# Kernel tuning notes

Hardware: AMD Instinct MI355X
Metric: run time of the kernel (lower is better)

The kernel has to match this reference:

```python
import jax, jax.numpy as jnp
import numpy as np

LAMBDA_SOFTMAX = 9.0
LAMBDA_LSE = 6.0
EPS = 1e-8
LEAKY_SLOPE = 0.1


def setup_inputs() -> dict:
    key = jax.random.key(0)
    k1, k2, k3, k4 = jax.random.split(key, 4)
    B, R, L, D = 256, 36, 40, 1024  # n_image=n_caption=B, n_regions, max_words, embed
    return {
        'pool_img': jax.random.normal(k1, (B, D), jnp.float32),
        'img_emb': jax.random.normal(k2, (B, R, D), jnp.float32),
        'pool_txt': jax.random.normal(k3, (B, D), jnp.float32),
        'cap_emb': jax.random.normal(k4, (B, L, D), jnp.float32),
    }


def _l2norm(x, axis):
    return x / (jnp.sqrt(jnp.sum(x * x, axis=axis, keepdims=True)) + EPS)


def _lse_reduce(m):
    # mul_(lambda_lse).exp_() ; sum over singleton dim ; log / lambda_lse
    return jnp.log(jnp.exp(m * LAMBDA_LSE)) / LAMBDA_LSE


def _text_score_one(cap_i, txt_poo_i, images):
    # cap_i: (L, d) query; images: (B, R, d) context. clipped_l2norm variant.
    attn = jnp.einsum('brd,ld->brl', images, cap_i)            # (B, R, L)
    attn = jax.nn.leaky_relu(attn, LEAKY_SLOPE)
    attn = _l2norm(attn, axis=2)                               # l2norm over queryL
    attn = jnp.swapaxes(attn, 1, 2)                            # (B, L, R)
    attn = jax.nn.softmax(attn * LAMBDA_SOFTMAX, axis=-1)      # softmax over regions
    wctx = jnp.einsum('blr,brd->bld', attn, images)            # (B, L, d)
    w12 = jnp.einsum('bld,d->bl', wctx, txt_poo_i)
    w1 = jnp.sqrt(jnp.sum(txt_poo_i * txt_poo_i))
    w2 = jnp.sqrt(jnp.sum(wctx * wctx, axis=2))
    sim = w12 / jnp.maximum(w1 * w2, EPS)                      # (B, L)
    return _lse_reduce(jnp.mean(sim, axis=1))                  # (B,)


def _image_score_one(cap_i, img_emb, img_poo):
    # query: img_emb (B, R, d); context: cap_i (L, d) broadcast over B.
    attn = jnp.einsum('ld,brd->blr', cap_i, img_emb)           # (B, L, R)
    attn = jax.nn.leaky_relu(attn, LEAKY_SLOPE)
    attn = _l2norm(attn, axis=2)                               # l2norm over regions
    attn = jnp.swapaxes(attn, 1, 2)                            # (B, R, L)
    attn = jax.nn.softmax(attn * LAMBDA_SOFTMAX, axis=-1)      # softmax over words
    wctx = jnp.einsum('brl,ld->brd', attn, cap_i)              # (B, R, d)
    w12 = jnp.einsum('brd,bd->br', wctx, img_poo)
    w1 = jnp.sqrt(jnp.sum(img_poo * img_poo, axis=1, keepdims=True))  # (B,1)
    w2 = jnp.sqrt(jnp.sum(wctx * wctx, axis=2))                # (B, R)
    sim = w12 / jnp.maximum(w1 * w2, EPS)
    return _lse_reduce(jnp.mean(sim, axis=1))                  # (B,)


def reference(pool_img, img_emb, pool_txt, cap_emb):
    # scores_t2i: loop over captions -> vmap; result (n_cap, n_image) -> transpose
    t2i = jax.vmap(_text_score_one, in_axes=(0, 0, None))(cap_emb, pool_txt, img_emb).T
    i2t = jax.vmap(_image_score_one, in_axes=(0, None, None))(cap_emb, img_emb, pool_img).T
    base = pool_img @ pool_txt.T
    return t2i + i2t + base
```

## Files before the change

kernel.cpp:

```cpp
#include <hip/hip_runtime.h>

typedef unsigned short u16;
typedef __attribute__((ext_vector_type(8))) short bf16x8;
typedef __attribute__((ext_vector_type(4))) float f32x4;

#define D_EMB 1024
#define NBAT  256
#define AS1 __attribute__((address_space(1)))
#define AS3 __attribute__((address_space(3)))

__device__ __forceinline__ u16 f2bf(float f){
    unsigned int u = __float_as_uint(f);
    unsigned int r = (u + 0x7fffu + ((u >> 16) & 1u)) >> 16;
    return (u16)r;
}
__device__ __forceinline__ float leaky(float x){ return x > 0.f ? x : 0.1f * x; }

__device__ __forceinline__ unsigned pack2(float a, float b){
    return (__float_as_uint(a) >> 16) | (__float_as_uint(b) & 0xffff0000u);
}
__device__ __forceinline__ float unpk_lo(unsigned p){ return __uint_as_float(p << 16); }
__device__ __forceinline__ float unpk_hi(unsigned p){ return __uint_as_float(p & 0xffff0000u); }

__global__ void pack_kernel(const float* __restrict__ pool_img, const float* __restrict__ img_emb,
                            const float* __restrict__ pool_txt, const float* __restrict__ cap_emb,
                            u16* __restrict__ imgw, u16* __restrict__ capw){
    int row = blockIdx.x;
    const float* src; u16* dst;
    if (row < NBAT * 37){
        int e = row / 37, rr = row - e * 37;
        src = (rr < 36) ? (img_emb + ((size_t)e * 36 + rr) * D_EMB) : (pool_img + (size_t)e * D_EMB);
        dst = imgw + (size_t)row * D_EMB;
    } else {
        int r2 = row - NBAT * 37;
        int e = r2 / 41, rr = r2 - e * 41;
        src = (rr < 40) ? (cap_emb + ((size_t)e * 40 + rr) * D_EMB) : (pool_txt + (size_t)e * D_EMB);
        dst = capw + (size_t)r2 * D_EMB;
    }
    int t = threadIdx.x;
    float4 v = ((const float4*)src)[t];
    unsigned long long pk = (unsigned long long)f2bf(v.x)
        | ((unsigned long long)f2bf(v.y) << 16)
        | ((unsigned long long)f2bf(v.z) << 32)
        | ((unsigned long long)f2bf(v.w) << 48);
    *(unsigned long long*)(dst + (size_t)t * 4) = pk;
}

__global__ void norm_kernel(const float* __restrict__ pool_img, const float* __restrict__ pool_txt,
                            float* __restrict__ w1i, float* __restrict__ w1t){
    __shared__ float red[256];
    int v = blockIdx.x;
    const float* src = (v < 256) ? (pool_img + (size_t)v * D_EMB)
                                 : (pool_txt + (size_t)(v - 256) * D_EMB);
    int t = threadIdx.x;
    float4 x = ((const float4*)src)[t];
    red[t] = x.x*x.x + x.y*x.y + x.z*x.z + x.w*x.w;
    __syncthreads();
    for (int off = 128; off > 0; off >>= 1){
        if (t < off) red[t] += red[t + off];
        __syncthreads();
    }
    if (t == 0){
        float n = sqrtf(red[0]);
        if (v < 256) w1i[v] = n; else w1t[v - 256] = n;
    }
}

__launch_bounds__(256, 2)
__global__ void gram_kernel(const u16* __restrict__ imgw, const u16* __restrict__ capw,
                            float* __restrict__ G, float* __restrict__ H){
    __shared__ __align__(16) char gsm[6144];
    int blk = blockIdx.x;
    int tid = threadIdx.x, lane = tid & 63;
    int wave = __builtin_amdgcn_readfirstlane(tid >> 6);
    int frow = lane & 15, q = lane >> 4;

    const u16* E; float* Gout; int R;
    if (blk < NBAT){ E = imgw + (size_t)blk * 37 * D_EMB; Gout = G + (size_t)blk * 1296; R = 36; }
    else { int b = blk - NBAT; E = capw + (size_t)b * 41 * D_EMB; Gout = H + (size_t)b * 1600; R = 40; }

    {
        uint4 z = {0u,0u,0u,0u};
        for (int off = tid * 16; off < 6144; off += 4096) *(uint4*)(gsm + off) = z;
    }

    const u16* gsrc[2]; int goff[2]; bool gval[2];
    #pragma unroll
    for (int j = 0; j < 2; ++j){
        int g = wave + j * 4;
        gval[j] = false; gsrc[j] = E; goff[j] = 0;
        if (g < 6){
            int kk = g / 3, t = g - kk * 3;
            int row = t * 16 + frow;
            gsrc[j] = E + (size_t)row * D_EMB + kk * 32 + q * 8;
            goff[j] = g * 1024;
            gval[j] = (row < R);
        }
    }

    int wm = wave >> 1, wn = wave & 1;
    int nTm = wm ? 1 : 2, nTn = wn ? 1 : 2;
    f32x4 acc[2][2];
    #pragma unroll
    for (int a = 0; a < 2; ++a)
        #pragma unroll
        for (int b = 0; b < 2; ++b) acc[a][b] = (f32x4){0.f,0.f,0.f,0.f};

    for (int c = 0; c < 16; ++c){
        __syncthreads();
        #pragma unroll
        for (int j = 0; j < 2; ++j){
            if (gval[j]){
                __builtin_amdgcn_global_load_lds(
                    (const AS1 void*)(const void*)(gsrc[j] + c * 64),
                    (AS3 void*)(void*)(gsm + goff[j] + lane * 16),
                    16, 0, 0);
            }
        }
        __syncthreads();
        #pragma unroll
        for (int kk = 0; kk < 2; ++kk){
            bf16x8 fA[2], fB[2];
            #pragma unroll
            for (int mi = 0; mi < 2; ++mi)
                if (mi < nTm) fA[mi] = *(const bf16x8*)(gsm + ((kk * 3 + (wm + mi * 2)) * 64 + lane) * 16);
            #pragma unroll
            for (int ni = 0; ni < 2; ++ni)
                if (ni < nTn) fB[ni] = *(const bf16x8*)(gsm + ((kk * 3 + (wn + ni * 2)) * 64 + lane) * 16);
            #pragma unroll
            for (int mi = 0; mi < 2; ++mi)
                if (mi < nTm)
                    #pragma unroll
                    for (int ni = 0; ni < 2; ++ni)
                        if (ni < nTn)
                            acc[mi][ni] = __builtin_amdgcn_mfma_f32_16x16x32_bf16(
                                fA[mi], fB[ni], acc[mi][ni], 0, 0, 0);
        }
    }

    #pragma unroll
    for (int mi = 0; mi < 2; ++mi){
        if (mi < nTm){
            int tm = wm + mi * 2;
            #pragma unroll
            for (int ni = 0; ni < 2; ++ni){
                if (ni < nTn){
                    int tn = wn + ni * 2;
                    int col = tn * 16 + frow;
                    if (col < R){
                        #pragma unroll
                        for (int g = 0; g < 4; ++g){
                            int row = tm * 16 + q * 4 + g;
                            if (row < R) Gout[row * R + col] = acc[mi][ni][g];
                        }
                    }
                }
            }
        }
    }
}

__launch_bounds__(256, 5)
__global__ void fused_kernel(const u16* __restrict__ imgw, const u16* __restrict__ capw,
                             const float* __restrict__ G, const float* __restrict__ H,
                             const float* __restrict__ w1i, const float* __restrict__ w1t,
                             float* __restrict__ out){
    __shared__ __align__(16) char smem[26624];
    float* Call = (float*)smem;
    float* rnb  = (float*)(smem + 25160);
    float* cnb  = (float*)(smem + 25736);

    int tid  = threadIdx.x;
    int lane = tid & 63;
    int wave = __builtin_amdgcn_readfirstlane(tid >> 6);
    int frow = lane & 15, q = lane >> 4;

    int lin = blockIdx.x;
    int xcd = lin & 7;
    int s   = lin >> 3;
    int b_t = (xcd << 4) | (s & 15);
    int i_t = s >> 4;
    int b0 = b_t * 2, i0 = i_t * 2;
    const u16* Ag = imgw + (size_t)b0 * 37 * D_EMB;
    const u16* Bg = capw + (size_t)i0 * 41 * D_EMB;

    {
        uint4 z = {0u,0u,0u,0u};
        for (int off = tid * 16; off < 22528; off += 4096) *(uint4*)(smem + off) = z;
    }

    const u16* gsrc[6]; int goff[6]; bool gval[6];
    #pragma unroll
    for (int j = 0; j < 6; ++j){
        int g = wave + j * 4;
        gval[j] = false; gsrc[j] = Ag; goff[j] = 0;
        if (g < 22){
            if (g < 10){
                int tm = g % 5, kk = g / 5;
                int row = tm * 16 + frow;
                gsrc[j] = Ag + (size_t)row * D_EMB + kk * 32 + q * 8;
                goff[j] = g * 1024;
                gval[j] = (row < 74);
            } else {
                int gb = g - 10;
                int tn = gb % 6, kk = gb / 6;
                int row = tn * 16 + frow;
                gsrc[j] = Bg + (size_t)row * D_EMB + kk * 32 + q * 8;
                goff[j] = 10240 + gb * 1024;
                gval[j] = (row < 82);
            }
        }
    }

    int wm = wave >> 1, wn = wave & 1;
    int nTm = wm ? 2 : 3;
    f32x4 acc[3][3];
    #pragma unroll
    for (int aa = 0; aa < 3; ++aa)
        #pragma unroll
        for (int bb = 0; bb < 3; ++bb) acc[aa][bb] = (f32x4){0.f, 0.f, 0.f, 0.f};

    for (int c = 0; c < 16; ++c){
        __syncthreads();
        #pragma unroll
        for (int j = 0; j < 6; ++j){
            if (gval[j]){
                __builtin_amdgcn_global_load_lds(
                    (const AS1 void*)(const void*)(gsrc[j] + c * 64),
                    (AS3 void*)(void*)(smem + goff[j] + lane * 16),
                    16, 0, 0);
            }
        }
        __syncthreads();
        #pragma unroll
        for (int kk = 0; kk < 2; ++kk){
            bf16x8 bfr[3];
            #pragma unroll
            for (int ni = 0; ni < 3; ++ni){
                int tn = wn + ni * 2;
                bfr[ni] = *(const bf16x8*)(smem + 10240 + ((kk * 6 + tn) * 64 + lane) * 16);
            }
            #pragma unroll
            for (int mi = 0; mi < 3; ++mi){
                if (mi < nTm){
                    int tm = wm + mi * 2;
                    bf16x8 af = *(const bf16x8*)(smem + ((kk * 5 + tm) * 64 + lane) * 16);
                    #pragma unroll
                    for (int ni = 0; ni < 3; ++ni){
                        acc[mi][ni] = __builtin_amdgcn_mfma_f32_16x16x32_bf16(
                            af, bfr[ni], acc[mi][ni], 0, 0, 0);
                    }
                }
            }
        }
    }
    __syncthreads();

    #pragma unroll
    for (int mi = 0; mi < 3; ++mi){
        if (mi < nTm){
            int tm = wm + mi * 2;
            #pragma unroll
            for (int ni = 0; ni < 3; ++ni){
                int tn = wn + ni * 2;
                int col = tn * 16 + frow;
                int rbase = tm * 16 + q * 4;
                if (col < 82){
                    #pragma unroll
                    for (int g = 0; g < 4; ++g){
                        int rowc = rbase + g;
                        if (rowc < 74) Call[rowc * 85 + col] = acc[mi][ni][g];
                    }
                }
            }
        }
    }
    __syncthreads();

    int pb = wave >> 1, pi = wave & 1;
    int bg = b0 + pb, ig = i0 + pi;
    const float* Sv = Call + (pb * 37) * 85 + pi * 41;
    const float* Gb = G + (size_t)bg * 1296;
    const float* Hi = H + (size_t)ig * 1600;

    {
        int r0 = (lane < 36) ? lane : 35;
        float s2 = 0.f;
        #pragma unroll
        for (int l = 0; l < 40; ++l){ float x = leaky(Sv[r0 * 85 + l]); s2 = fmaf(x, x, s2); }
        if (lane < 36) rnb[wave * 36 + lane] = 1.f / (sqrtf(s2) + 1e-8f);
    }
    float t2i_sum;
    {
        int lc = (lane < 40) ? lane : 39;
        unsigned up[18];
        float dd = 0.f, num = 0.f;
        #pragma unroll
        for (int r = 0; r < 36; r += 2){
            float x0 = leaky(Sv[r * 85 + lc]);
            float e0 = __expf(9.0f * x0 * rnb[wave * 36 + r]);
            float x1 = leaky(Sv[(r + 1) * 85 + lc]);
            float e1 = __expf(9.0f * x1 * rnb[wave * 36 + r + 1]);
            dd += e0 + e1;
            num = fmaf(e0, Sv[r * 85 + 40], fmaf(e1, Sv[(r + 1) * 85 + 40], num));
            up[r >> 1] = pack2(e0, e1);
        }
        float zz = 0.f;
        #pragma unroll
        for (int rr = 0; rr < 36; ++rr){
            float urr = (rr & 1) ? unpk_hi(up[rr >> 1]) : unpk_lo(up[rr >> 1]);
            float t = 0.f;
            #pragma unroll
            for (int r2 = rr + 1; r2 < 36; ++r2){
                float ur2 = (r2 & 1) ? unpk_hi(up[r2 >> 1]) : unpk_lo(up[r2 >> 1]);
                t = fmaf(Gb[rr * 36 + r2], ur2, t);
            }
            zz += (2.f * t + Gb[rr * 36 + rr] * urr) * urr;
        }
        float w2s = sqrtf(fmaxf(zz, 0.f));
        float sim = num / fmaxf(w1t[ig] * w2s, 1e-8f);
        sim = (lane < 40) ? sim : 0.f;
        #pragma unroll
        for (int off = 32; off > 0; off >>= 1) sim += __shfl_down(sim, off);
        t2i_sum = sim;
    }

    {
        int l0 = (lane < 40) ? lane : 39;
        float s2 = 0.f;
        #pragma unroll
        for (int r = 0; r < 36; ++r){ float x = leaky(Sv[r * 85 + l0]); s2 = fmaf(x, x, s2); }
        if (lane < 40) cnb[wave * 40 + lane] = 1.f / (sqrtf(s2) + 1e-8f);
    }
    float i2t_sum;
    {
        int rc = (lane < 36) ? lane : 35;
        unsigned vp[20];
        float dd = 0.f, num = 0.f;
        #pragma unroll
        for (int l = 0; l < 40; l += 2){
            float x0 = leaky(Sv[rc * 85 + l]);
            float e0 = __expf(9.0f * x0 * cnb[wave * 40 + l]);
            float x1 = leaky(Sv[rc * 85 + l + 1]);
            float e1 = __expf(9.0f * x1 * cnb[wave * 40 + l + 1]);
            dd += e0 + e1;
            num = fmaf(e0, Sv[36 * 85 + l], fmaf(e1, Sv[36 * 85 + l + 1], num));
            vp[l >> 1] = pack2(e0, e1);
        }
        float zz = 0.f;
        #pragma unroll
        for (int ll = 0; ll < 40; ++ll){
            float vll = (ll & 1) ? unpk_hi(vp[ll >> 1]) : unpk_lo(vp[ll >> 1]);
            float t = 0.f;
            #pragma unroll
            for (int l2 = ll + 1; l2 < 40; ++l2){
                float vl2 = (l2 & 1) ? unpk_hi(vp[l2 >> 1]) : unpk_lo(vp[l2 >> 1]);
                t = fmaf(Hi[ll * 40 + l2], vl2, t);
            }
            zz += (2.f * t + Hi[ll * 40 + ll] * vll) * vll;
        }
        float w2s = sqrtf(fmaxf(zz, 0.f));
        float sim = num / fmaxf(w1i[bg] * w2s, 1e-8f);
        sim = (lane < 36) ? sim : 0.f;
        #pragma unroll
        for (int off = 32; off > 0; off >>= 1) sim += __shfl_down(sim, off);
        i2t_sum = sim;
    }

    if (lane == 0)
        out[bg * 256 + ig] = t2i_sum * (1.f / 40.f) + i2t_sum * (1.f / 36.f) + Sv[36 * 85 + 40];
}

extern "C" void kernel_launch(void* const* d_in, const int* in_sizes, int n_in,
                              void* d_out, int out_size, void* d_ws, size_t ws_size,
                              hipStream_t stream){
    const float* pool_img = (const float*)d_in[0];
    const float* img_emb  = (const float*)d_in[1];
    const float* pool_txt = (const float*)d_in[2];
    const float* cap_emb  = (const float*)d_in[3];
    float* out = (float*)d_out;

    char* ws = (char*)d_ws;
    size_t o = 0;
    u16* imgw = (u16*)(ws + o);  o += (size_t)256 * 37 * 1024 * 2;
    u16* capw = (u16*)(ws + o);  o += (size_t)256 * 41 * 1024 * 2;
    float* G  = (float*)(ws + o); o += (size_t)256 * 36 * 36 * 4;
    float* H  = (float*)(ws + o); o += (size_t)256 * 40 * 40 * 4;
    float* w1i = (float*)(ws + o); o += 1024;
    float* w1t = (float*)(ws + o); o += 1024;

    pack_kernel<<<19968, 256, 0, stream>>>(pool_img, img_emb, pool_txt, cap_emb, imgw, capw);
    norm_kernel<<<512, 256, 0, stream>>>(pool_img, pool_txt, w1i, w1t);
    gram_kernel<<<512, 256, 0, stream>>>(imgw, capw, G, H);
    fused_kernel<<<16384, 256, 0, stream>>>(imgw, capw, G, H, w1i, w1t, out);
}
```

Before: 753.4 us.

## Compute softmax-weight quadratic forms with MFMA against bf16-padded Gram matrices

The per-lane scalar quadratic form u^T G u (and v^T H v), which read fp32 Gram entries from global memory inside a triangular unrolled loop, is replaced by MFMA products. The Gram matrices are stored as zero-padded 48x64 bf16 tiles, and the packed exp weights are staged through a per-wave LDS buffer as the B operand. This cuts the scalar FMA count and the global load traffic in the hot epilogue. In exchange it adds LDS staging, bf16 rounding of G/H, a larger shared-memory footprint that may reduce occupancy, and reliance on compiler-only barriers for intra-wave LDS ordering.

```diff
diff --git a/kernel.cpp b/kernel.cpp
--- a/kernel.cpp
+++ b/kernel.cpp
@@ -8,6 +8,7 @@
 #define NBAT  256
 #define AS1 __attribute__((address_space(1)))
 #define AS3 __attribute__((address_space(3)))
+#define MEMBAR() asm volatile("" ::: "memory")
 
 __device__ __forceinline__ u16 f2bf(float f){
     unsigned int u = __float_as_uint(f);
@@ -68,19 +69,23 @@
 
 __launch_bounds__(256, 2)
 __global__ void gram_kernel(const u16* __restrict__ imgw, const u16* __restrict__ capw,
-                            float* __restrict__ G, float* __restrict__ H){
+                            u16* __restrict__ Gp, u16* __restrict__ Hp){
     __shared__ __align__(16) char gsm[6144];
     int blk = blockIdx.x;
     int tid = threadIdx.x, lane = tid & 63;
     int wave = __builtin_amdgcn_readfirstlane(tid >> 6);
     int frow = lane & 15, q = lane >> 4;
 
-    const u16* E; float* Gout; int R;
-    if (blk < NBAT){ E = imgw + (size_t)blk * 37 * D_EMB; Gout = G + (size_t)blk * 1296; R = 36; }
-    else { int b = blk - NBAT; E = capw + (size_t)b * 41 * D_EMB; Gout = H + (size_t)b * 1600; R = 40; }
-
-    {
-        uint4 z = {0u,0u,0u,0u};
+    const u16* E; u16* Gout; int R;
+    if (blk < NBAT){ E = imgw + (size_t)blk * 37 * D_EMB; Gout = Gp + (size_t)blk * 3072; R = 36; }
+    else { int b = blk - NBAT; E = capw + (size_t)b * 41 * D_EMB; Gout = Hp + (size_t)b * 3072; R = 40; }
+
+    for (int idx = tid; idx < 3072; idx += 256){
+        int row = idx >> 6, col = idx & 63;
+        if (row >= R || col >= R) Gout[idx] = 0;
+    }
+
+    {   uint4 z = {0u,0u,0u,0u};
         for (int off = tid * 16; off < 6144; off += 4096) *(uint4*)(gsm + off) = z;
     }
 
@@ -151,7 +156,7 @@
                         #pragma unroll
                         for (int g = 0; g < 4; ++g){
                             int row = tm * 16 + q * 4 + g;
-                            if (row < R) Gout[row * R + col] = acc[mi][ni][g];
+                            if (row < R) Gout[row * 64 + col] = f2bf(acc[mi][ni][g]);
                         }
                     }
                 }
@@ -162,13 +167,11 @@
 
 __launch_bounds__(256, 5)
 __global__ void fused_kernel(const u16* __restrict__ imgw, const u16* __restrict__ capw,
-                             const float* __restrict__ G, const float* __restrict__ H,
+                             const u16* __restrict__ Gp, const u16* __restrict__ Hp,
                              const float* __restrict__ w1i, const float* __restrict__ w1t,
                              float* __restrict__ out){
-    __shared__ __align__(16) char smem[26624];
+    __shared__ __align__(16) char smem[32768];
     float* Call = (float*)smem;
-    float* rnb  = (float*)(smem + 25160);
-    float* cnb  = (float*)(smem + 25736);
 
     int tid  = threadIdx.x;
     int lane = tid & 63;
@@ -187,6 +190,8 @@
     {
         uint4 z = {0u,0u,0u,0u};
         for (int off = tid * 16; off < 22528; off += 4096) *(uint4*)(smem + off) = z;
+        *(uint4*)(smem + 24576 + tid * 32)      = z;
+        *(uint4*)(smem + 24576 + tid * 32 + 16) = z;
     }
 
     const u16* gsrc[6]; int goff[6]; bool gval[6];
@@ -269,7 +274,7 @@
                     #pragma unroll
                     for (int g = 0; g < 4; ++g){
                         int rowc = rbase + g;
-                        if (rowc < 74) Call[rowc * 85 + col] = acc[mi][ni][g];
+                        if (rowc < 74) Call[rowc * 83 + col] = acc[mi][ni][g];
                     }
                 }
             }
@@ -279,88 +284,155 @@
 
     int pb = wave >> 1, pi = wave & 1;
     int bg = b0 + pb, ig = i0 + pi;
-    const float* Sv = Call + (pb * 37) * 85 + pi * 41;
-    const float* Gb = G + (size_t)bg * 1296;
-    const float* Hi = H + (size_t)ig * 1600;
+    const float* Sv = Call + (pb * 37) * 83 + pi * 41;
+    const u16* Gb = Gp + (size_t)bg * 3072;
+    const u16* Hb = Hp + (size_t)ig * 3072;
+    char*  pbuf  = smem + 24576 + wave * 2048;
+    float* pnorm = (float*)pbuf;
+
+    float t2i_sum, i2t_sum;
 
     {
         int r0 = (lane < 36) ? lane : 35;
         float s2 = 0.f;
         #pragma unroll
-        for (int l = 0; l < 40; ++l){ float x = leaky(Sv[r0 * 85 + l]); s2 = fmaf(x, x, s2); }
-        if (lane < 36) rnb[wave * 36 + lane] = 1.f / (sqrtf(s2) + 1e-8f);
-    }
-    float t2i_sum;
+        for (int l = 0; l < 40; ++l){ float x = leaky(Sv[r0 * 83 + l]); s2 = fmaf(x, x, s2); }
+        if (lane < 36) pnorm[lane] = 1.f / (sqrtf(s2) + 1e-8f);
+        MEMBAR();
+    }
     {
         int lc = (lane < 40) ? lane : 39;
         unsigned up[18];
-        float dd = 0.f, num = 0.f;
+        float num = 0.f;
         #pragma unroll
         for (int r = 0; r < 36; r += 2){
-            float x0 = leaky(Sv[r * 85 + lc]);
-            float e0 = __expf(9.0f * x0 * rnb[wave * 36 + r]);
-            float x1 = leaky(Sv[(r + 1) * 85 + lc]);
-            float e1 = __expf(9.0f * x1 * rnb[wave * 36 + r + 1]);
-            dd += e0 + e1;
-            num = fmaf(e0, Sv[r * 85 + 40], fmaf(e1, Sv[(r + 1) * 85 + 40], num));
+            float x0 = leaky(Sv[r * 83 + lc]);
+            float e0 = __expf(9.0f * x0 * pnorm[r]);
+            float x1 = leaky(Sv[(r + 1) * 83 + lc]);
+            float e1 = __expf(9.0f * x1 * pnorm[r + 1]);
+            num = fmaf(e0, Sv[r * 83 + 40], fmaf(e1, Sv[(r + 1) * 83 + 40], num));
             up[r >> 1] = pack2(e0, e1);
         }
-        float zz = 0.f;
-        #pragma unroll
-        for (int rr = 0; rr < 36; ++rr){
-            float urr = (rr & 1) ? unpk_hi(up[rr >> 1]) : unpk_lo(up[rr >> 1]);
-            float t = 0.f;
-            #pragma unroll
-            for (int r2 = rr + 1; r2 < 36; ++r2){
-                float ur2 = (r2 & 1) ? unpk_hi(up[r2 >> 1]) : unpk_lo(up[r2 >> 1]);
-                t = fmaf(Gb[rr * 36 + r2], ur2, t);
-            }
-            zz += (2.f * t + Gb[rr * 36 + rr] * urr) * urr;
-        }
-        float w2s = sqrtf(fmaxf(zz, 0.f));
-        float sim = num / fmaxf(w1t[ig] * w2s, 1e-8f);
+        MEMBAR();
+        float zzp[3];
+        #pragma unroll
+        for (int ni = 0; ni < 3; ++ni){
+            if (lane < 40 && (lane >> 4) == ni){
+                int fr = lane & 15;
+                #pragma unroll
+                for (int qq = 0; qq < 4; ++qq){
+                    uint4 w = {up[qq * 4], up[qq * 4 + 1], up[qq * 4 + 2], up[qq * 4 + 3]};
+                    *(uint4*)(pbuf + (qq * 16 + fr) * 16) = w;
+                }
+                uint4 w1 = {up[16], up[17], 0u, 0u};
+                *(uint4*)(pbuf + 1024 + fr * 16) = w1;
+            }
+            MEMBAR();
+            uint4 tb0 = *(const uint4*)(pbuf + lane * 16);
+            uint4 tb1 = *(const uint4*)(pbuf + 1024 + lane * 16);
+            bf16x8 B0 = __builtin_bit_cast(bf16x8, tb0);
+            bf16x8 B1 = __builtin_bit_cast(bf16x8, tb1);
+            float zp = 0.f;
+            #pragma unroll
+            for (int mi = 0; mi < 3; ++mi){
+                bf16x8 A0 = *(const bf16x8*)(Gb + (mi * 16 + frow) * 64 + q * 8);
+                bf16x8 A1 = *(const bf16x8*)(Gb + (mi * 16 + frow) * 64 + 32 + q * 8);
+                f32x4 w = (f32x4){0.f, 0.f, 0.f, 0.f};
+                w = __builtin_amdgcn_mfma_f32_16x16x32_bf16(A0, B0, w, 0, 0, 0);
+                w = __builtin_amdgcn_mfma_f32_16x16x32_bf16(A1, B1, w, 0, 0, 0);
+                int k0 = mi * 16 + q * 4;
+                int kc = k0 >> 5, km = k0 & 31;
+                uint2 ud = *(const uint2*)(pbuf + kc * 1024 + ((km >> 3) * 16 + frow) * 16 + (q & 1) * 8);
+                zp = fmaf(w[0], unpk_lo(ud.x), zp);
+                zp = fmaf(w[1], unpk_hi(ud.x), zp);
+                zp = fmaf(w[2], unpk_lo(ud.y), zp);
+                zp = fmaf(w[3], unpk_hi(ud.y), zp);
+            }
+            zzp[ni] = zp;
+            MEMBAR();
+        }
+        #pragma unroll
+        for (int ni = 0; ni < 3; ++ni){
+            zzp[ni] += __shfl_xor(zzp[ni], 16);
+            zzp[ni] += __shfl_xor(zzp[ni], 32);
+        }
+        int sel = lc >> 4;
+        float zz = (sel == 0) ? zzp[0] : ((sel == 1) ? zzp[1] : zzp[2]);
+        float sim = num / fmaxf(w1t[ig] * sqrtf(fmaxf(zz, 0.f)), 1e-8f);
         sim = (lane < 40) ? sim : 0.f;
         #pragma unroll
         for (int off = 32; off > 0; off >>= 1) sim += __shfl_down(sim, off);
         t2i_sum = sim;
     }
 
+    MEMBAR();
     {
         int l0 = (lane < 40) ? lane : 39;
         float s2 = 0.f;
         #pragma unroll
-        for (int r = 0; r < 36; ++r){ float x = leaky(Sv[r * 85 + l0]); s2 = fmaf(x, x, s2); }
-        if (lane < 40) cnb[wave * 40 + lane] = 1.f / (sqrtf(s2) + 1e-8f);
-    }
-    float i2t_sum;
+        for (int r = 0; r < 36; ++r){ float x = leaky(Sv[r * 83 + l0]); s2 = fmaf(x, x, s2); }
+        if (lane < 40) pnorm[lane] = 1.f / (sqrtf(s2) + 1e-8f);
+        MEMBAR();
+    }
     {
         int rc = (lane < 36) ? lane : 35;
         unsigned vp[20];
-        float dd = 0.f, num = 0.f;
+        float num = 0.f;
         #pragma unroll
         for (int l = 0; l < 40; l += 2){
-            float x0 = leaky(Sv[rc * 85 + l]);
-            float e0 = __expf(9.0f * x0 * cnb[wave * 40 + l]);
-            float x1 = leaky(Sv[rc * 85 + l + 1]);
-            float e1 = __expf(9.0f * x1 * cnb[wave * 40 + l + 1]);
-            dd += e0 + e1;
-            num = fmaf(e0, Sv[36 * 85 + l], fmaf(e1, Sv[36 * 85 + l + 1], num));
+            float x0 = leaky(Sv[rc * 83 + l]);
+            float e0 = __expf(9.0f * x0 * pnorm[l]);
+            float x1 = leaky(Sv[rc * 83 + l + 1]);
+            float e1 = __expf(9.0f * x1 * pnorm[l + 1]);
+            num = fmaf(e0, Sv[36 * 83 + l], fmaf(e1, Sv[36 * 83 + l + 1], num));
             vp[l >> 1] = pack2(e0, e1);
         }
-        float zz = 0.f;
-        #pragma unroll
-        for (int ll = 0; ll < 40; ++ll){
-            float vll = (ll & 1) ? unpk_hi(vp[ll >> 1]) : unpk_lo(vp[ll >> 1]);
-            float t = 0.f;
-            #pragma unroll
-            for (int l2 = ll + 1; l2 < 40; ++l2){
-                float vl2 = (l2 & 1) ? unpk_hi(vp[l2 >> 1]) : unpk_lo(vp[l2 >> 1]);
-                t = fmaf(Hi[ll * 40 + l2], vl2, t);
-            }
-            zz += (2.f * t + Hi[ll * 40 + ll] * vll) * vll;
-        }
-        float w2s = sqrtf(fmaxf(zz, 0.f));
-        float sim = num / fmaxf(w1i[bg] * w2s, 1e-8f);
+        MEMBAR();
+        float zzp[3];
+        #pragma unroll
+        for (int ni = 0; ni < 3; ++ni){
+            if (lane < 36 && (lane >> 4) == ni){
+                int fr = lane & 15;
+                #pragma unroll
+                for (int qq = 0; qq < 4; ++qq){
+                    uint4 w = {vp[qq * 4], vp[qq * 4 + 1], vp[qq * 4 + 2], vp[qq * 4 + 3]};
+                    *(uint4*)(pbuf + (qq * 16 + fr) * 16) = w;
+                }
+                uint4 w1 = {vp[16], vp[17], vp[18], vp[19]};
+                *(uint4*)(pbuf + 1024 + fr * 16) = w1;
+            }
+            MEMBAR();
+            uint4 tb0 = *(const uint4*)(pbuf + lane * 16);
+            uint4 tb1 = *(const uint4*)(pbuf + 1024 + lane * 16);
+            bf16x8 B0 = __builtin_bit_cast(bf16x8, tb0);
+            bf16x8 B1 = __builtin_bit_cast(bf16x8, tb1);
+            float zp = 0.f;
+            #pragma unroll
+            for (int mi = 0; mi < 3; ++mi){
+                bf16x8 A0 = *(const bf16x8*)(Hb + (mi * 16 + frow) * 64 + q * 8);
+                bf16x8 A1 = *(const bf16x8*)(Hb + (mi * 16 + frow) * 64 + 32 + q * 8);
+                f32x4 w = (f32x4){0.f, 0.f, 0.f, 0.f};
+                w = __builtin_amdgcn_mfma_f32_16x16x32_bf16(A0, B0, w, 0, 0, 0);
+                w = __builtin_amdgcn_mfma_f32_16x16x32_bf16(A1, B1, w, 0, 0, 0);
+                int k0 = mi * 16 + q * 4;
+                int kc = k0 >> 5, km = k0 & 31;
+                uint2 ud = *(const uint2*)(pbuf + kc * 1024 + ((km >> 3) * 16 + frow) * 16 + (q & 1) * 8);
+                zp = fmaf(w[0], unpk_lo(ud.x), zp);
+                zp = fmaf(w[1], unpk_hi(ud.x), zp);
+                zp = fmaf(w[2], unpk_lo(ud.y), zp);
+                zp = fmaf(w[3], unpk_hi(ud.y), zp);
+            }
+            zzp[ni] = zp;
+            MEMBAR();
+        }
+        #pragma unroll
+        for (int ni = 0; ni < 3; ++ni){
+            zzp[ni] += __shfl_xor(zzp[ni], 16);
+            zzp[ni] += __shfl_xor(zzp[ni], 32);
+        }
+        int sel = rc >> 4;
+        float zz = (sel == 0) ? zzp[0] : ((sel == 1) ? zzp[1] : zzp[2]);
+        float sim = num / fmaxf(w1i[bg] * sqrtf(fmaxf(zz, 0.f)), 1e-8f);
         sim = (lane < 36) ? sim : 0.f;
         #pragma unroll
         for (int off = 32; off > 0; off >>= 1) sim += __shfl_down(sim, off);
@@ -368,7 +440,7 @@
     }
 
     if (lane == 0)
-        out[bg * 256 + ig] = t2i_sum * (1.f / 40.f) + i2t_sum * (1.f / 36.f) + Sv[36 * 85 + 40];
+        out[bg * 256 + ig] = t2i_sum * (1.f / 40.f) + i2t_sum * (1.f / 36.f) + Sv[36 * 83 + 40];
 }
 
 extern "C" void kernel_launch(void* const* d_in, const int* in_sizes, int n_in,
@@ -384,13 +456,13 @@
     size_t o = 0;
     u16* imgw = (u16*)(ws + o);  o += (size_t)256 * 37 * 1024 * 2;
     u16* capw = (u16*)(ws + o);  o += (size_t)256 * 41 * 1024 * 2;
-    float* G  = (float*)(ws + o); o += (size_t)256 * 36 * 36 * 4;
-    float* H  = (float*)(ws + o); o += (size_t)256 * 40 * 40 * 4;
+    u16* Gp   = (u16*)(ws + o);  o += (size_t)256 * 48 * 64 * 2;
+    u16* Hp   = (u16*)(ws + o);  o += (size_t)256 * 48 * 64 * 2;
     float* w1i = (float*)(ws + o); o += 1024;
     float* w1t = (float*)(ws + o); o += 1024;
 
     pack_kernel<<<19968, 256, 0, stream>>>(pool_img, img_emb, pool_txt, cap_emb, imgw, capw);
     norm_kernel<<<512, 256, 0, stream>>>(pool_img, pool_txt, w1i, w1t);
-    gram_kernel<<<512, 256, 0, stream>>>(imgw, capw, G, H);
-    fused_kernel<<<16384, 256, 0, stream>>>(imgw, capw, G, H, w1i, w1t, out);
-}
+    gram_kernel<<<512, 256, 0, stream>>>(imgw, capw, Gp, Hp);
+    fused_kernel<<<16384, 256, 0, stream>>>(imgw, capw, Gp, Hp, w1i, w1t, out);
+}
```

After: 1.363 ms. 80.9% more time.
